# Optimization experiments

Measured on AMD Instinct MI355X. Metric: run time of the kernel, lower is better.

## Reference

```python
import jax, jax.numpy as jnp
import numpy as np

EMB = 2048
HEADS = 8
HEAD_DIM = EMB // HEADS  # 256

def setup_inputs() -> dict:
    key = jax.random.key(0)
    ks = jax.random.split(key, 4)
    b, n = 2, 2048
    x = jax.random.normal(ks[0], (b, n, EMB), dtype=jnp.float32)
    # Linear weights stored as [in, out] (y = x @ W + b)
    w_qkv = jax.random.normal(ks[1], (EMB, 3 * EMB), dtype=jnp.float32) * (EMB ** -0.5)
    b_qkv = jnp.zeros((3 * EMB,), dtype=jnp.float32)
    w_proj = jax.random.normal(ks[2], (EMB, EMB), dtype=jnp.float32) * (EMB ** -0.5)
    b_proj = jnp.zeros((EMB,), dtype=jnp.float32)
    return {"x": x, "w_qkv": w_qkv, "b_qkv": b_qkv, "w_proj": w_proj, "b_proj": b_proj}

def reference(x, w_qkv, b_qkv, w_proj, b_proj):
    b, n, _ = x.shape
    qkv = x @ w_qkv + b_qkv                                   # [b, n, 3*emb]
    # rearrange 'b n (h d qkv) -> qkv b h n d': qkv index is innermost
    qkv = qkv.reshape(b, n, HEADS, HEAD_DIM, 3)
    qkv = jnp.transpose(qkv, (4, 0, 2, 1, 3))                 # [3, b, h, n, d]
    q, k, v = qkv[0], qkv[1], qkv[2]
    energy = jnp.einsum('bhqd,bhkd->bhqk', q, k)              # [b, h, n, n]
    scaling = EMB ** 0.5
    # NOTE: faithful to source — softmax on UNSCALED logits, divide after.
    att = jax.nn.softmax(energy, axis=-1) / scaling
    out = jnp.einsum('bhal,bhlv->bhav', att, v)               # [b, h, n, d]
    out = jnp.transpose(out, (0, 2, 1, 3)).reshape(b, n, EMB)  # b n (h d)
    return out @ w_proj + b_proj
```

## Files before the change

### kernel.cpp

```cpp
#include <hip/hip_runtime.h>
#include <cstdint>
#include <cstddef>


typedef __bf16 bf16x8 __attribute__((ext_vector_type(8)));
typedef __bf16 bf16x2 __attribute__((ext_vector_type(2)));
typedef float f32x4 __attribute__((ext_vector_type(4)));

#define SCALE_INV 0.022097086912079608f

__device__ inline void split8(const float4 v0, const float4 v1, bf16x8& hi,
                              bf16x8& lo) {
  float a[8] = {v0.x, v0.y, v0.z, v0.w, v1.x, v1.y, v1.z, v1.w};
  bf16x8 h, l;
#pragma unroll
  for (int i = 0; i < 8; i++) {
    __bf16 hh = (__bf16)a[i];
    h[i] = hh;
    l[i] = (__bf16)(a[i] - (float)hh);
  }
  hi = h;
  lo = l;
}

__global__ __launch_bounds__(256) void transpose_cvt_k(
    const float* __restrict__ in, __bf16* __restrict__ out, int R, int C) {
  __shared__ float tile[32][33];
  const int tx = threadIdx.x & 31;
  const int ty = threadIdx.x >> 5;
  const int c0 = blockIdx.x * 32;
  const int r0 = blockIdx.y * 32;
#pragma unroll
  for (int i = 0; i < 32; i += 8)
    tile[ty + i][tx] = in[(size_t)(r0 + ty + i) * C + (c0 + tx)];
  __syncthreads();
#pragma unroll
  for (int i = 0; i < 32; i += 8)
    out[(size_t)(c0 + ty + i) * R + (r0 + tx)] = (__bf16)tile[tx][ty + i];
}

__global__ __launch_bounds__(256) void gemm_qkv_split_k(
    const float* __restrict__ X, const float* __restrict__ W,
    const float* __restrict__ bias, __bf16* __restrict__ qh_,
    __bf16* __restrict__ ql_, __bf16* __restrict__ kh_,
    __bf16* __restrict__ kl_, __bf16* __restrict__ vT) {
  __shared__ __bf16 Ah[128 * 40], Al[128 * 40];
  __shared__ __bf16 Bh[128 * 40], Bl[128 * 40];
  const int tid = threadIdx.x, lane = tid & 63, wave = tid >> 6;
  const int l16 = lane & 15, quad = lane >> 4;
  const int wm = (wave >> 1) * 64, wn = (wave & 1) * 64;
  const int m0 = blockIdx.y * 128, n0 = blockIdx.x * 128;
  const int r0 = tid >> 2, kc0 = (tid & 3) * 8;
  const int bn = tid & 31;
  const int bk = (tid >> 5) * 2;

  f32x4 zero4 = {0.f, 0.f, 0.f, 0.f};
  f32x4 acc[4][4];
#pragma unroll
  for (int i = 0; i < 4; i++)
#pragma unroll
    for (int j = 0; j < 4; j++) acc[i][j] = zero4;

  const float* Arow0 = X + (size_t)(m0 + r0) * 2048 + kc0;
  const float* Arow1 = Arow0 + (size_t)64 * 2048;

  for (int k0 = 0; k0 < 2048; k0 += 32) {
    float4 a00 = *(const float4*)(Arow0 + k0);
    float4 a01 = *(const float4*)(Arow0 + k0 + 4);
    float4 a10 = *(const float4*)(Arow1 + k0);
    float4 a11 = *(const float4*)(Arow1 + k0 + 4);
    float wv[2][4][2];
#pragma unroll
    for (int p = 0; p < 2; p++) {
      const int kk = k0 + p * 16 + bk;
#pragma unroll
      for (int i = 0; i < 4; i++) {
        const int nn = n0 + bn + 32 * i;
        wv[p][i][0] = W[(size_t)kk * 6144 + nn];
        wv[p][i][1] = W[(size_t)(kk + 1) * 6144 + nn];
      }
    }
    bf16x8 ah0, al0, ah1, al1;
    split8(a00, a01, ah0, al0);
    split8(a10, a11, ah1, al1);
    __syncthreads();
    *(bf16x8*)&Ah[r0 * 40 + kc0] = ah0;
    *(bf16x8*)&Al[r0 * 40 + kc0] = al0;
    *(bf16x8*)&Ah[(r0 + 64) * 40 + kc0] = ah1;
    *(bf16x8*)&Al[(r0 + 64) * 40 + kc0] = al1;
#pragma unroll
    for (int p = 0; p < 2; p++) {
      const int kk = p * 16 + bk;
#pragma unroll
      for (int i = 0; i < 4; i++) {
        const int nn = bn + 32 * i;
        const float a = wv[p][i][0], b = wv[p][i][1];
        __bf16 h0 = (__bf16)a, h1 = (__bf16)b;
        bf16x2 h = {h0, h1};
        bf16x2 l = {(__bf16)(a - (float)h0), (__bf16)(b - (float)h1)};
        *(bf16x2*)&Bh[nn * 40 + kk] = h;
        *(bf16x2*)&Bl[nn * 40 + kk] = l;
      }
    }
    __syncthreads();
    bf16x8 fah[4], fal[4], fbh[4], fbl[4];
#pragma unroll
    for (int i = 0; i < 4; i++) {
      fah[i] = *(const bf16x8*)&Ah[(wm + i * 16 + l16) * 40 + quad * 8];
      fal[i] = *(const bf16x8*)&Al[(wm + i * 16 + l16) * 40 + quad * 8];
    }
#pragma unroll
    for (int j = 0; j < 4; j++) {
      fbh[j] = *(const bf16x8*)&Bh[(wn + j * 16 + l16) * 40 + quad * 8];
      fbl[j] = *(const bf16x8*)&Bl[(wn + j * 16 + l16) * 40 + quad * 8];
    }
#pragma unroll
    for (int i = 0; i < 4; i++)
#pragma unroll
      for (int j = 0; j < 4; j++) {
        acc[i][j] = __builtin_amdgcn_mfma_f32_16x16x32_bf16(fah[i], fbh[j],
                                                            acc[i][j], 0, 0, 0);
        acc[i][j] = __builtin_amdgcn_mfma_f32_16x16x32_bf16(fah[i], fbl[j],
                                                            acc[i][j], 0, 0, 0);
        acc[i][j] = __builtin_amdgcn_mfma_f32_16x16x32_bf16(fal[i], fbh[j],
                                                            acc[i][j], 0, 0, 0);
      }
  }

#pragma unroll
  for (int i = 0; i < 4; i++) {
#pragma unroll
    for (int j = 0; j < 4; j++) {
      const int col = n0 + wn + j * 16 + l16;
      const float bv = bias[col];
      const int h = col / 768;
      const int rr = col - h * 768;
      const int d = rr / 3;
      const int c = rr - d * 3;
#pragma unroll
      for (int r = 0; r < 4; r++) {
        const int row = m0 + wm + i * 16 + quad * 4 + r;
        const float v = acc[i][j][r] + bv;
        const int b = row >> 11;
        const int nn = row & 2047;
        const int bh = b * 8 + h;
        const size_t idx = ((size_t)bh * 2048 + nn) * 256 + d;
        if (c == 0) {
          __bf16 hi = (__bf16)v;
          qh_[idx] = hi;
          ql_[idx] = (__bf16)(v - (float)hi);
        } else if (c == 1) {
          __bf16 hi = (__bf16)v;
          kh_[idx] = hi;
          kl_[idx] = (__bf16)(v - (float)hi);
        } else {
          vT[((size_t)bh * 256 + d) * 2048 + nn] = (__bf16)v;
        }
      }
    }
  }
}

#define GLDS16(gp, lp)                                                        \
  __builtin_amdgcn_global_load_lds(                                           \
      (const __attribute__((address_space(1))) void*)(gp),                    \
      (__attribute__((address_space(3))) void*)(lp), 16, 0, 0)

__global__ __launch_bounds__(256, 2) void attn_fwd_k(
    const __bf16* __restrict__ Qh,
    const __bf16* __restrict__ Ql,
    const __bf16* __restrict__ Kh,
    const __bf16* __restrict__ Kl,
    const __bf16* __restrict__ Vt,
    __bf16* __restrict__ out) {
  __shared__ __attribute__((aligned(16))) __bf16 KhL[64 * 256];
  __shared__ __attribute__((aligned(16))) __bf16 KlL[64 * 256];
  __shared__ __attribute__((aligned(16))) __bf16 Plds[4][16 * 72];

  const int qblk = blockIdx.x;
  const int bh = blockIdx.y;
  const int bb = bh >> 3, hh = bh & 7;
  const int tid = threadIdx.x, lane = tid & 63, wave = tid >> 6;
  const int l16 = lane & 15, quad = lane >> 4;

  const size_t hqk = (size_t)bh * 2048 * 256;
  const __bf16* qhp = Qh + hqk;
  const __bf16* qlp = Ql + hqk;
  const __bf16* khp = Kh + hqk;
  const __bf16* klp = Kl + hqk;
  const __bf16* vp = Vt + (size_t)bh * 256 * 2048;

  const int qrow = qblk * 64 + wave * 16;

  bf16x8 qhf[8], qlf[8];
#pragma unroll
  for (int t = 0; t < 8; t++) {
    const size_t off = (size_t)(qrow + l16) * 256 + t * 32 + quad * 8;
    qhf[t] = *(const bf16x8*)&qhp[off];
    qlf[t] = *(const bf16x8*)&qlp[off];
  }

  f32x4 zero4 = {0.f, 0.f, 0.f, 0.f};
  f32x4 o[16];
#pragma unroll
  for (int dt = 0; dt < 16; dt++) o[dt] = zero4;
  float mrow[4], lrow[4];
#pragma unroll
  for (int r = 0; r < 4; r++) {
    mrow[r] = -3.0e38f;
    lrow[r] = 0.f;
  }

  int koff[8];
#pragma unroll
  for (int i = 0; i < 8; i++) {
    const int r = wave * 16 + i * 2 + (lane >> 5);
    const int cb = ((lane & 31) << 4) ^ ((r & 7) << 4);
    koff[i] = r * 256 + (cb >> 1);
  }
  const int ldsb = wave * 4096;

#pragma unroll
  for (int i = 0; i < 8; i++) {
    GLDS16(khp + koff[i], &KhL[ldsb + i * 512]);
    GLDS16(klp + koff[i], &KlL[ldsb + i * 512]);
  }

  for (int kv0 = 0; kv0 < 2048; kv0 += 64) {
    __syncthreads();

    f32x4 s[4];
#pragma unroll
    for (int j = 0; j < 4; j++) s[j] = zero4;
    __builtin_amdgcn_s_setprio(1);
#pragma unroll
    for (int j = 0; j < 4; j++) {
      const int row = j * 16 + l16;
      const int swz = (row & 7) << 3;
      const int rb = row * 256;
#pragma unroll
      for (int t = 0; t < 8; t++) {
        const int off = rb + ((t * 32 + quad * 8) ^ swz);
        bf16x8 khf = *(const bf16x8*)&KhL[off];
        bf16x8 klf = *(const bf16x8*)&KlL[off];
        s[j] =
            __builtin_amdgcn_mfma_f32_16x16x32_bf16(qhf[t], khf, s[j], 0, 0, 0);
        s[j] =
            __builtin_amdgcn_mfma_f32_16x16x32_bf16(qhf[t], klf, s[j], 0, 0, 0);
        s[j] =
            __builtin_amdgcn_mfma_f32_16x16x32_bf16(qlf[t], khf, s[j], 0, 0, 0);
      }
    }
    __builtin_amdgcn_s_setprio(0);
    __syncthreads();

    if (kv0 + 64 < 2048) {
      const int kvn = (kv0 + 64) * 256;
#pragma unroll
      for (int i = 0; i < 8; i++) {
        GLDS16(khp + kvn + koff[i], &KhL[ldsb + i * 512]);
        GLDS16(klp + kvn + koff[i], &KlL[ldsb + i * 512]);
      }
    }

    float mnew[4], alpha[4], psum[4];
#pragma unroll
    for (int r = 0; r < 4; r++) {
      float mx = fmaxf(fmaxf(s[0][r], s[1][r]), fmaxf(s[2][r], s[3][r]));
#pragma unroll
      for (int off = 1; off < 16; off <<= 1)
        mx = fmaxf(mx, __shfl_xor(mx, off, 16));
      mnew[r] = fmaxf(mrow[r], mx);
      alpha[r] = __expf(mrow[r] - mnew[r]);
      psum[r] = 0.f;
    }
#pragma unroll
    for (int j = 0; j < 4; j++)
#pragma unroll
      for (int r = 0; r < 4; r++) {
        float p = __expf(s[j][r] - mnew[r]);
        s[j][r] = p;
        psum[r] += p;
      }
#pragma unroll
    for (int r = 0; r < 4; r++) {
#pragma unroll
      for (int off = 1; off < 16; off <<= 1)
        psum[r] += __shfl_xor(psum[r], off, 16);
      lrow[r] = lrow[r] * alpha[r] + psum[r];
      mrow[r] = mnew[r];
    }
#pragma unroll
    for (int dt = 0; dt < 16; dt++) {
      o[dt][0] *= alpha[0];
      o[dt][1] *= alpha[1];
      o[dt][2] *= alpha[2];
      o[dt][3] *= alpha[3];
    }
#pragma unroll
    for (int j = 0; j < 4; j++)
#pragma unroll
      for (int r = 0; r < 4; r++)
        Plds[wave][(quad * 4 + r) * 72 + j * 16 + l16] = (__bf16)s[j][r];
    bf16x8 pa0 = *(const bf16x8*)&Plds[wave][l16 * 72 + quad * 8];
    bf16x8 pa1 = *(const bf16x8*)&Plds[wave][l16 * 72 + 32 + quad * 8];

    __builtin_amdgcn_s_setprio(1);
#pragma unroll
    for (int dt = 0; dt < 16; dt++) {
      const __bf16* vr = vp + (size_t)(dt * 16 + l16) * 2048 + kv0 + quad * 8;
      bf16x8 vf0 = *(const bf16x8*)vr;
      bf16x8 vf1 = *(const bf16x8*)(vr + 32);
      o[dt] = __builtin_amdgcn_mfma_f32_16x16x32_bf16(pa0, vf0, o[dt], 0, 0, 0);
      o[dt] = __builtin_amdgcn_mfma_f32_16x16x32_bf16(pa1, vf1, o[dt], 0, 0, 0);
    }
    __builtin_amdgcn_s_setprio(0);
  }

#pragma unroll
  for (int r = 0; r < 4; r++) {
    const float inv = SCALE_INV / lrow[r];
    const int n = qrow + quad * 4 + r;
    const size_t base = ((size_t)bb * 2048 + n) * 2048 + hh * 256;
#pragma unroll
    for (int dt = 0; dt < 16; dt++)
      out[base + dt * 16 + l16] = (__bf16)(o[dt][r] * inv);
  }
}

__global__ __launch_bounds__(256) void gemm_bt_k(
    const __bf16* __restrict__ A, const __bf16* __restrict__ Bt,
    const float* __restrict__ bias, int M, int Ncols, int K,
    float* __restrict__ outF) {
  __shared__ __bf16 As[128 * 40];
  __shared__ __bf16 Bs[128 * 40];
  const int tid = threadIdx.x, lane = tid & 63, wave = tid >> 6;
  const int l16 = lane & 15, quad = lane >> 4;
  const int wm = (wave >> 1) * 64, wn = (wave & 1) * 64;
  const int m0 = blockIdx.y * 128, n0 = blockIdx.x * 128;
  const int r0 = tid >> 2, kc0 = (tid & 3) * 8;

  f32x4 zero4 = {0.f, 0.f, 0.f, 0.f};
  f32x4 acc[4][4];
#pragma unroll
  for (int i = 0; i < 4; i++)
#pragma unroll
    for (int j = 0; j < 4; j++) acc[i][j] = zero4;

  const __bf16* Aptr = A + (size_t)(m0 + r0) * K + kc0;
  const __bf16* Bptr = Bt + (size_t)(n0 + r0) * K + kc0;
  const size_t rowstep = (size_t)64 * K;

  for (int k0 = 0; k0 < K; k0 += 32) {
    uint4 a0 = *(const uint4*)(Aptr + k0);
    uint4 a1 = *(const uint4*)(Aptr + rowstep + k0);
    uint4 b0 = *(const uint4*)(Bptr + k0);
    uint4 b1 = *(const uint4*)(Bptr + rowstep + k0);
    __syncthreads();
    *(uint4*)&As[r0 * 40 + kc0] = a0;
    *(uint4*)&As[(r0 + 64) * 40 + kc0] = a1;
    *(uint4*)&Bs[r0 * 40 + kc0] = b0;
    *(uint4*)&Bs[(r0 + 64) * 40 + kc0] = b1;
    __syncthreads();
    bf16x8 af[4], bfv[4];
#pragma unroll
    for (int i = 0; i < 4; i++)
      af[i] = *(const bf16x8*)&As[(wm + i * 16 + l16) * 40 + quad * 8];
#pragma unroll
    for (int j = 0; j < 4; j++)
      bfv[j] = *(const bf16x8*)&Bs[(wn + j * 16 + l16) * 40 + quad * 8];
#pragma unroll
    for (int i = 0; i < 4; i++)
#pragma unroll
      for (int j = 0; j < 4; j++)
        acc[i][j] = __builtin_amdgcn_mfma_f32_16x16x32_bf16(af[i], bfv[j],
                                                            acc[i][j], 0, 0, 0);
  }

#pragma unroll
  for (int i = 0; i < 4; i++)
#pragma unroll
    for (int j = 0; j < 4; j++) {
      const int col = n0 + wn + j * 16 + l16;
      const float bv = bias[col];
#pragma unroll
      for (int r = 0; r < 4; r++) {
        const int row = m0 + wm + i * 16 + quad * 4 + r;
        outF[(size_t)row * Ncols + col] = acc[i][j][r] + bv;
      }
    }
}

extern "C" void kernel_launch(void* const* d_in, const int* in_sizes, int n_in,
                              void* d_out, int out_size, void* d_ws,
                              size_t ws_size, hipStream_t stream) {
  const float* x = (const float*)d_in[0];
  const float* w_qkv = (const float*)d_in[1];
  const float* b_qkv = (const float*)d_in[2];
  const float* w_proj = (const float*)d_in[3];
  const float* b_proj = (const float*)d_in[4];
  float* out = (float*)d_out;

  const size_t HSZ = (size_t)16 * 2048 * 256;
  __bf16* qh = (__bf16*)d_ws;
  __bf16* ql = qh + HSZ;
  __bf16* kh = ql + HSZ;
  __bf16* kl = kh + HSZ;
  __bf16* vT = kl + HSZ;
  __bf16* attn = vT + HSZ;
  __bf16* wprojT = qh;

  gemm_qkv_split_k<<<dim3(48, 32), 256, 0, stream>>>(x, w_qkv, b_qkv, qh, ql,
                                                     kh, kl, vT);
  attn_fwd_k<<<dim3(32, 16), 256, 0, stream>>>(qh, ql, kh, kl, vT, attn);
  transpose_cvt_k<<<dim3(64, 64), 256, 0, stream>>>(w_proj, wprojT, 2048, 2048);
  gemm_bt_k<<<dim3(16, 32), 256, 0, stream>>>(attn, wprojT, b_proj, 4096, 2048,
                                              2048, out);
}
```

Measured before the change: 940.9 us.

## Pre-split QKV weights to bf16 hi/lo and double-buffer GEMM B tiles via LDS DMA

Adds a pre-pass kernel that transposes w_qkv and splits it into bf16 hi/lo planes, stored in scratch space borrowed from the output and attention buffers. The QKV GEMM then streams B tiles straight into swizzled, double-buffered LDS with global_load_lds and prefetches the next A tile while the MFMAs run. Block indices are also remapped to improve cache locality. This removes the strided fp32 weight gathers and per-tile conversion inside the GEMM loop, at the cost of an extra kernel launch and the memory traffic of writing and re-reading the bf16 weights.

```diff
diff --git a/kernel.cpp b/kernel.cpp
--- a/kernel.cpp
+++ b/kernel.cpp
@@ -8,6 +8,11 @@
 typedef float f32x4 __attribute__((ext_vector_type(4)));
 
 #define SCALE_INV 0.022097086912079608f
+
+#define GLDS16(gp, lp)                                                        \
+  __builtin_amdgcn_global_load_lds(                                           \
+      (const __attribute__((address_space(1))) void*)(gp),                    \
+      (__attribute__((address_space(3))) void*)(lp), 16, 0, 0)
 
 __device__ inline void split8(const float4 v0, const float4 v1, bf16x8& hi,
                               bf16x8& lo) {
@@ -39,20 +44,57 @@
     out[(size_t)(c0 + ty + i) * R + (r0 + tx)] = (__bf16)tile[tx][ty + i];
 }
 
+__global__ __launch_bounds__(256) void transpose_w_split_k(
+    const float* __restrict__ in, __bf16* __restrict__ wh,
+    __bf16* __restrict__ wl1, __bf16* __restrict__ wl2) {
+  __shared__ float tile[64][65];
+  const int tid = threadIdx.x;
+  const int c0 = blockIdx.x * 64;
+  const int r0 = blockIdx.y * 64;
+  const int cx = tid & 15, ry = tid >> 4;
+#pragma unroll
+  for (int p = 0; p < 4; p++) {
+    const float4 v =
+        *(const float4*)&in[(size_t)(r0 + p * 16 + ry) * 6144 + c0 + cx * 4];
+    tile[p * 16 + ry][cx * 4 + 0] = v.x;
+    tile[p * 16 + ry][cx * 4 + 1] = v.y;
+    tile[p * 16 + ry][cx * 4 + 2] = v.z;
+    tile[p * 16 + ry][cx * 4 + 3] = v.w;
+  }
+  __syncthreads();
+  const int r2 = tid & 31;
+  const int cy = tid >> 5;
+  __bf16* wlb = (c0 < 2048) ? wl1 + (size_t)c0 * 2048
+                            : wl2 + (size_t)(c0 - 2048) * 2048;
+#pragma unroll
+  for (int p = 0; p < 8; p++) {
+    const int cl = cy + p * 8;
+    const float t0 = tile[2 * r2][cl];
+    const float t1 = tile[2 * r2 + 1][cl];
+    const __bf16 h0 = (__bf16)t0, h1 = (__bf16)t1;
+    bf16x2 hv = {h0, h1};
+    bf16x2 lv = {(__bf16)(t0 - (float)h0), (__bf16)(t1 - (float)h1)};
+    *(bf16x2*)&wh[(size_t)(c0 + cl) * 2048 + r0 + 2 * r2] = hv;
+    *(bf16x2*)&wlb[(size_t)cl * 2048 + r0 + 2 * r2] = lv;
+  }
+}
+
 __global__ __launch_bounds__(256) void gemm_qkv_split_k(
-    const float* __restrict__ X, const float* __restrict__ W,
+    const float* __restrict__ X, const __bf16* __restrict__ Wh,
+    const __bf16* __restrict__ Wl1, const __bf16* __restrict__ Wl2,
     const float* __restrict__ bias, __bf16* __restrict__ qh_,
     __bf16* __restrict__ ql_, __bf16* __restrict__ kh_,
     __bf16* __restrict__ kl_, __bf16* __restrict__ vT) {
   __shared__ __bf16 Ah[128 * 40], Al[128 * 40];
-  __shared__ __bf16 Bh[128 * 40], Bl[128 * 40];
+  __shared__ __attribute__((aligned(16))) __bf16 BhL[2 * 4096];
+  __shared__ __attribute__((aligned(16))) __bf16 BlL[2 * 4096];
   const int tid = threadIdx.x, lane = tid & 63, wave = tid >> 6;
   const int l16 = lane & 15, quad = lane >> 4;
   const int wm = (wave >> 1) * 64, wn = (wave & 1) * 64;
-  const int m0 = blockIdx.y * 128, n0 = blockIdx.x * 128;
+  const int bid = blockIdx.y * 48 + blockIdx.x;
+  const int nb2 = (bid & 7) * 192 + (bid >> 3);
+  const int m0 = (nb2 / 48) * 128, n0 = (nb2 % 48) * 128;
   const int r0 = tid >> 2, kc0 = (tid & 3) * 8;
-  const int bn = tid & 31;
-  const int bk = (tid >> 5) * 2;
 
   f32x4 zero4 = {0.f, 0.f, 0.f, 0.f};
   f32x4 acc[4][4];
@@ -63,46 +105,54 @@
 
   const float* Arow0 = X + (size_t)(m0 + r0) * 2048 + kc0;
   const float* Arow1 = Arow0 + (size_t)64 * 2048;
+  const __bf16* BhP = Wh + (size_t)n0 * 2048;
+  const __bf16* BlP = (n0 < 2048) ? Wl1 + (size_t)n0 * 2048
+                                  : Wl2 + (size_t)(n0 - 2048) * 2048;
+
+  const int rowl = lane >> 2, gq = lane & 3;
+  const int sg = gq ^ (rowl & 3);
+  size_t bSrc[2];
+  int bDst[2];
+#pragma unroll
+  for (int i = 0; i < 2; i++) {
+    const int row = wave * 32 + i * 16 + rowl;
+    bSrc[i] = (size_t)row * 2048 + sg * 8;
+    bDst[i] = (wave * 32 + i * 16) * 32;
+  }
+  const int bro = (wn + l16) * 32 + ((quad ^ (l16 & 3)) << 3);
+
+  GLDS16(BhP + bSrc[0], &BhL[bDst[0]]);
+  GLDS16(BhP + bSrc[1], &BhL[bDst[1]]);
+  GLDS16(BlP + bSrc[0], &BlL[bDst[0]]);
+  GLDS16(BlP + bSrc[1], &BlL[bDst[1]]);
+  float4 a00 = *(const float4*)(Arow0);
+  float4 a01 = *(const float4*)(Arow0 + 4);
+  float4 a10 = *(const float4*)(Arow1);
+  float4 a11 = *(const float4*)(Arow1 + 4);
+  bf16x8 ah0, al0, ah1, al1;
+  split8(a00, a01, ah0, al0);
+  split8(a10, a11, ah1, al1);
+  *(bf16x8*)&Ah[r0 * 40 + kc0] = ah0;
+  *(bf16x8*)&Al[r0 * 40 + kc0] = al0;
+  *(bf16x8*)&Ah[(r0 + 64) * 40 + kc0] = ah1;
+  *(bf16x8*)&Al[(r0 + 64) * 40 + kc0] = al1;
 
   for (int k0 = 0; k0 < 2048; k0 += 32) {
-    float4 a00 = *(const float4*)(Arow0 + k0);
-    float4 a01 = *(const float4*)(Arow0 + k0 + 4);
-    float4 a10 = *(const float4*)(Arow1 + k0);
-    float4 a11 = *(const float4*)(Arow1 + k0 + 4);
-    float wv[2][4][2];
-#pragma unroll
-    for (int p = 0; p < 2; p++) {
-      const int kk = k0 + p * 16 + bk;
-#pragma unroll
-      for (int i = 0; i < 4; i++) {
-        const int nn = n0 + bn + 32 * i;
-        wv[p][i][0] = W[(size_t)kk * 6144 + nn];
-        wv[p][i][1] = W[(size_t)(kk + 1) * 6144 + nn];
-      }
-    }
-    bf16x8 ah0, al0, ah1, al1;
-    split8(a00, a01, ah0, al0);
-    split8(a10, a11, ah1, al1);
+    const int cur = (k0 >> 5) & 1;
+    const int cb = cur * 4096;
     __syncthreads();
-    *(bf16x8*)&Ah[r0 * 40 + kc0] = ah0;
-    *(bf16x8*)&Al[r0 * 40 + kc0] = al0;
-    *(bf16x8*)&Ah[(r0 + 64) * 40 + kc0] = ah1;
-    *(bf16x8*)&Al[(r0 + 64) * 40 + kc0] = al1;
-#pragma unroll
-    for (int p = 0; p < 2; p++) {
-      const int kk = p * 16 + bk;
-#pragma unroll
-      for (int i = 0; i < 4; i++) {
-        const int nn = bn + 32 * i;
-        const float a = wv[p][i][0], b = wv[p][i][1];
-        __bf16 h0 = (__bf16)a, h1 = (__bf16)b;
-        bf16x2 h = {h0, h1};
-        bf16x2 l = {(__bf16)(a - (float)h0), (__bf16)(b - (float)h1)};
-        *(bf16x2*)&Bh[nn * 40 + kk] = h;
-        *(bf16x2*)&Bl[nn * 40 + kk] = l;
-      }
-    }
-    __syncthreads();
+    const int nxt = k0 + 32;
+    if (nxt < 2048) {
+      const int nb = (cur ^ 1) * 4096;
+      GLDS16(BhP + bSrc[0] + nxt, &BhL[nb + bDst[0]]);
+      GLDS16(BhP + bSrc[1] + nxt, &BhL[nb + bDst[1]]);
+      GLDS16(BlP + bSrc[0] + nxt, &BlL[nb + bDst[0]]);
+      GLDS16(BlP + bSrc[1] + nxt, &BlL[nb + bDst[1]]);
+      a00 = *(const float4*)(Arow0 + nxt);
+      a01 = *(const float4*)(Arow0 + nxt + 4);
+      a10 = *(const float4*)(Arow1 + nxt);
+      a11 = *(const float4*)(Arow1 + nxt + 4);
+    }
     bf16x8 fah[4], fal[4], fbh[4], fbl[4];
 #pragma unroll
     for (int i = 0; i < 4; i++) {
@@ -111,8 +161,8 @@
     }
 #pragma unroll
     for (int j = 0; j < 4; j++) {
-      fbh[j] = *(const bf16x8*)&Bh[(wn + j * 16 + l16) * 40 + quad * 8];
-      fbl[j] = *(const bf16x8*)&Bl[(wn + j * 16 + l16) * 40 + quad * 8];
+      fbh[j] = *(const bf16x8*)&BhL[cb + bro + j * 512];
+      fbl[j] = *(const bf16x8*)&BlL[cb + bro + j * 512];
     }
 #pragma unroll
     for (int i = 0; i < 4; i++)
@@ -125,6 +175,15 @@
         acc[i][j] = __builtin_amdgcn_mfma_f32_16x16x32_bf16(fal[i], fbh[j],
                                                             acc[i][j], 0, 0, 0);
       }
+    if (nxt < 2048) {
+      split8(a00, a01, ah0, al0);
+      split8(a10, a11, ah1, al1);
+      __syncthreads();
+      *(bf16x8*)&Ah[r0 * 40 + kc0] = ah0;
+      *(bf16x8*)&Al[r0 * 40 + kc0] = al0;
+      *(bf16x8*)&Ah[(r0 + 64) * 40 + kc0] = ah1;
+      *(bf16x8*)&Al[(r0 + 64) * 40 + kc0] = al1;
+    }
   }
 
 #pragma unroll
@@ -161,11 +220,6 @@
   }
 }
 
-#define GLDS16(gp, lp)                                                        \
-  __builtin_amdgcn_global_load_lds(                                           \
-      (const __attribute__((address_space(1))) void*)(gp),                    \
-      (__attribute__((address_space(3))) void*)(lp), 16, 0, 0)
-
 __global__ __launch_bounds__(256, 2) void attn_fwd_k(
     const __bf16* __restrict__ Qh,
     const __bf16* __restrict__ Ql,
@@ -410,8 +464,13 @@
   __bf16* attn = vT + HSZ;
   __bf16* wprojT = qh;
 
-  gemm_qkv_split_k<<<dim3(48, 32), 256, 0, stream>>>(x, w_qkv, b_qkv, qh, ql,
-                                                     kh, kl, vT);
+  __bf16* wh = (__bf16*)out;
+  __bf16* wl1 = wh + (size_t)6144 * 2048;
+  __bf16* wl2 = attn;
+
+  transpose_w_split_k<<<dim3(96, 32), 256, 0, stream>>>(w_qkv, wh, wl1, wl2);
+  gemm_qkv_split_k<<<dim3(48, 32), 256, 0, stream>>>(x, wh, wl1, wl2, b_qkv,
+                                                     qh, ql, kh, kl, vT);
   attn_fwd_k<<<dim3(32, 16), 256, 0, stream>>>(qh, ql, kh, kl, vT, attn);
   transpose_cvt_k<<<dim3(64, 64), 256, 0, stream>>>(w_proj, wprojT, 2048, 2048);
   gemm_bt_k<<<dim3(16, 32), 256, 0, stream>>>(attn, wprojT, b_proj, 4096, 2048,
```

After: 973.5 us. 1.03x slower.
